# Kernel optimization log

Measured on AMD Instinct MI355X. Metric: run time of the kernel, lower is better.

The kernel has to match this reference:

```python
import jax, jax.numpy as jnp
import numpy as np

B, S, V, E, H, L = 128, 512, 32000, 256, 256, 9


def setup_inputs() -> dict:
    key = jax.random.key(0)
    ks = jax.random.split(key, 12)
    src_input = jax.random.randint(ks[0], (B, S), 0, V, dtype=jnp.int32)
    labels = jax.random.randint(ks[1], (B, S), 0, L, dtype=jnp.int32)
    masks = jnp.ones((B, S), dtype=bool)  # torchcrf requires mask[:, 0] all True
    g = lambda k, shape, s: (jax.random.normal(k, shape, jnp.float32) * s)
    inv = 1.0 / np.sqrt(H)
    return {
        "src_input": src_input,
        "labels": labels,
        "masks": masks,
        "embedding": g(ks[2], (V, E), 0.1),
        "W_ih": g(ks[3], (4 * H, E), inv),
        "W_hh": g(ks[4], (4 * H, H), inv),
        "b_ih": g(ks[5], (4 * H,), inv),
        "b_hh": g(ks[6], (4 * H,), inv),
        "W_lin": g(ks[7], (L, H), inv),
        "b_lin": g(ks[8], (L,), inv),
        "start_trans": g(ks[9], (L,), 0.1),
        "end_trans": g(ks[10], (L,), 0.1),
        "trans": g(ks[11], (L, L), 0.1),
    }


def _lstm(x, W_ih, W_hh, b_ih, b_hh):
    # x: [B,S,E] -> hidden states [B,S,H]; PyTorch gate order i,f,g,o
    b, s, _ = x.shape
    h_dim = W_hh.shape[1]
    xp = jnp.einsum('bse,ge->sbg', x, W_ih) + b_ih  # [S,B,4H] precomputed input proj

    def step(carry, xt):
        h, c = carry
        gates = xt + h @ W_hh.T + b_hh
        i, f, g, o = jnp.split(gates, 4, axis=-1)
        c = jax.nn.sigmoid(f) * c + jax.nn.sigmoid(i) * jnp.tanh(g)
        h = jax.nn.sigmoid(o) * jnp.tanh(c)
        return (h, c), h

    h0 = jnp.zeros((b, h_dim), x.dtype)
    _, hs = jax.lax.scan(step, (h0, h0), xp)  # [S,B,H]
    return jnp.swapaxes(hs, 0, 1)


def _crf_nll(emissions, labels, masks, start_trans, end_trans, trans):
    # torchcrf log-likelihood (reduction='sum'); model returns its negation
    maskf = masks.astype(emissions.dtype)
    lab = labels.astype(jnp.int32)
    # numerator: score of gold path
    em_tag = jnp.take_along_axis(emissions, lab[..., None], axis=2)[..., 0]  # [B,S]
    trans_sc = trans[lab[:, :-1], lab[:, 1:]]  # [B,S-1]
    score = start_trans[lab[:, 0]] + em_tag[:, 0]
    score = score + jnp.sum((trans_sc + em_tag[:, 1:]) * maskf[:, 1:], axis=1)
    seq_ends = jnp.sum(masks.astype(jnp.int32), axis=1) - 1
    last_tags = jnp.take_along_axis(lab, seq_ends[:, None], axis=1)[:, 0]
    score = score + end_trans[last_tags]
    # denominator: forward algorithm (log partition)
    alpha0 = start_trans + emissions[:, 0]  # [B,L]
    em_t = jnp.swapaxes(emissions, 0, 1)[1:]  # [S-1,B,L]
    m_t = jnp.swapaxes(masks, 0, 1)[1:]  # [S-1,B]

    def step(alpha, inp):
        e, m = inp
        nxt = jax.nn.logsumexp(alpha[:, :, None] + trans[None] + e[:, None, :], axis=1)
        return jnp.where(m[:, None], nxt, alpha), None

    alphaT, _ = jax.lax.scan(step, alpha0, (em_t, m_t))
    logZ = jax.nn.logsumexp(alphaT + end_trans, axis=1)  # [B]
    return -jnp.sum(score - logZ)


def reference(src_input, labels, masks, embedding, W_ih, W_hh, b_ih, b_hh,
              W_lin, b_lin, start_trans, end_trans, trans):
    x = embedding[src_input]  # [B,S,E]
    hs = _lstm(x, W_ih, W_hh, b_ih, b_hh)  # [B,S,H]; dropout is identity in eval
    emissions = jax.nn.relu(hs) @ W_lin.T + b_lin  # [B,S,L]
    return _crf_nll(emissions, labels, masks, start_trans, end_trans, trans)
```

## Files before the change

### kernel.cpp

```cpp
#include <hip/hip_runtime.h>
#include <hip/hip_fp16.h>
#include <stdint.h>

#define B_ 128
#define S_ 512
#define E_ 256
#define H_ 256
#define G_ 1024
#define L_ 9

#define NREG 45
#define NLDS 19
#define WREG_U4 (NREG * 512)
#define WTOT_U4 (WREG_U4 + NLDS * 512)

#define SM_H2   155648
#define SMEM2_TOTAL 156672

#define WS_W      0
#define WS_XP     (512 * 1024)
#define WS_HS     (WS_XP + (size_t)S_ * B_ * G_ * 2)
#define WS_EMB16  (WS_HS + (size_t)S_ * B_ * H_ * 2)
#define WS_WIH16  (WS_EMB16 + (size_t)32000 * E_ * 2)

typedef _Float16 f16x8v __attribute__((ext_vector_type(8)));
typedef float    f32x4v __attribute__((ext_vector_type(4)));

__device__ __forceinline__ uint32_t pack_f16x2(float a, float b) {
    __half2 h = __floats2half2_rn(a, b);
    union { __half2 h2; uint32_t u; } c;
    c.h2 = h;
    return c.u;
}

__device__ __forceinline__ float dot2h(uint32_t w, uint32_t h, float acc) {
#if __has_builtin(__builtin_amdgcn_fdot2)
    typedef _Float16 h2v __attribute__((ext_vector_type(2)));
    union { uint32_t u; h2v v; } uw, uh;
    uw.u = w; uh.u = h;
    return __builtin_amdgcn_fdot2(uw.v, uh.v, acc, false);
#else
    union { uint32_t u; __half2 h2; } uw, uh;
    uw.u = w; uh.u = h;
    float2 wf = __half22float2(uw.h2);
    float2 hf = __half22float2(uh.h2);
    return fmaf(wf.y, hf.y, fmaf(wf.x, hf.x, acc));
#endif
}

__device__ __forceinline__ float dot4h(uint4 w, uint4 h, float acc) {
    acc = dot2h(w.x, h.x, acc);
    acc = dot2h(w.y, h.y, acc);
    acc = dot2h(w.z, h.z, acc);
    acc = dot2h(w.w, h.w, acc);
    return acc;
}

__device__ __forceinline__ float sigm(float x)  { return 1.f / (1.f + __expf(-x)); }
__device__ __forceinline__ float tanh_f(float x){ return 1.f - 2.f / (__expf(2.f * x) + 1.f); }

__device__ __forceinline__ void lds_barrier() {
    asm volatile("s_waitcnt lgkmcnt(0)\n\ts_barrier" ::: "memory");
}

__global__ __launch_bounds__(256) void prep_weights(const float* __restrict__ W_hh,
                                                    uint4* __restrict__ W) {
    int idx = blockIdx.x * 256 + threadIdx.x;
    int l, w, q;
    if (idx < WREG_U4) {
        l = idx & 63; w = (idx >> 6) & 7; q = idx >> 9;
    } else {
        int r = idx - WREG_U4;
        l = r & 63; w = (r >> 6) & 7; q = NREG + (r >> 9);
    }
    int kt = q >> 3, nt = q & 7;
    int gate = nt & 3, jbl = nt >> 2;
    int jb = 2 * w + jbl;
    int row = gate * 256 + jb * 16 + (l & 15);
    int col = kt * 32 + (l >> 4) * 8;
    const float* p = W_hh + (size_t)row * H_ + col;
    uint4 v;
    v.x = pack_f16x2(p[0], p[1]);
    v.y = pack_f16x2(p[2], p[3]);
    v.z = pack_f16x2(p[4], p[5]);
    v.w = pack_f16x2(p[6], p[7]);
    W[idx] = v;
}

__global__ __launch_bounds__(256) void cvt_f16(const float* __restrict__ in,
                                               uint4* __restrict__ out, int n8) {
    int i = blockIdx.x * 256 + threadIdx.x;
    if (i >= n8) return;
    const float4* p = (const float4*)(in + (size_t)i * 8);
    float4 a = p[0], b = p[1];
    uint4 v;
    v.x = pack_f16x2(a.x, a.y);
    v.y = pack_f16x2(a.z, a.w);
    v.z = pack_f16x2(b.x, b.y);
    v.w = pack_f16x2(b.z, b.w);
    out[i] = v;
}

#define PADK 40
__global__ __launch_bounds__(256) void xp_gemm_mfma(
    const int* __restrict__ src, const __half* __restrict__ emb16,
    const __half* __restrict__ wih16, const float* __restrict__ b_ih,
    const float* __restrict__ b_hh, __half* __restrict__ xp16)
{
    __shared__ __align__(16) __half A_lds[64 * PADK];
    __shared__ __align__(16) __half Bt_lds[64 * PADK];
    __shared__ __align__(16) __half C_lds[64 * 72];
    __shared__ int tok[64];
    __shared__ float bias[64];

    int tid = threadIdx.x;
    int r0  = blockIdx.x * 64;
    int j0  = blockIdx.y * 16;

    if (tid < 64) {
        int r = r0 + tid;
        int tt = r >> 7, bb = r & 127;
        tok[tid] = src[bb * S_ + tt];
        int grow = (tid >> 4) * 256 + j0 + (tid & 15);
        bias[tid] = b_ih[grow] + b_hh[grow];
    }
    __syncthreads();

    int row = tid >> 2, q = tid & 3;
    const __half* arow = emb16 + (size_t)tok[row] * E_ + q * 8;
    int growb = (row >> 4) * 256 + j0 + (row & 15);
    const __half* brow = wih16 + (size_t)growb * E_ + q * 8;
    __half* asl = &A_lds[row * PADK + q * 8];
    __half* bsl = &Bt_lds[row * PADK + q * 8];

    int lane = tid & 63, w = tid >> 6;
    int ln = lane & 15, quad = lane >> 4;

    f32x4v acc0 = {0.f, 0.f, 0.f, 0.f};
    f32x4v acc1 = {0.f, 0.f, 0.f, 0.f};
    f32x4v acc2 = {0.f, 0.f, 0.f, 0.f};
    f32x4v acc3 = {0.f, 0.f, 0.f, 0.f};

    for (int kc = 0; kc < E_; kc += 32) {
        *(uint4*)asl = *(const uint4*)(arow + kc);
        *(uint4*)bsl = *(const uint4*)(brow + kc);
        __syncthreads();
        f16x8v af  = *(const f16x8v*)&A_lds[(w * 16 + ln) * PADK + quad * 8];
        f16x8v bf0 = *(const f16x8v*)&Bt_lds[(ln)      * PADK + quad * 8];
        f16x8v bf1 = *(const f16x8v*)&Bt_lds[(16 + ln) * PADK + quad * 8];
        f16x8v bf2 = *(const f16x8v*)&Bt_lds[(32 + ln) * PADK + quad * 8];
        f16x8v bf3 = *(const f16x8v*)&Bt_lds[(48 + ln) * PADK + quad * 8];
        acc0 = __builtin_amdgcn_mfma_f32_16x16x32_f16(af, bf0, acc0, 0, 0, 0);
        acc1 = __builtin_amdgcn_mfma_f32_16x16x32_f16(af, bf1, acc1, 0, 0, 0);
        acc2 = __builtin_amdgcn_mfma_f32_16x16x32_f16(af, bf2, acc2, 0, 0, 0);
        acc3 = __builtin_amdgcn_mfma_f32_16x16x32_f16(af, bf3, acc3, 0, 0, 0);
        __syncthreads();
    }

    #pragma unroll
    for (int nt = 0; nt < 4; ++nt) {
        f32x4v a = (nt == 0) ? acc0 : (nt == 1) ? acc1 : (nt == 2) ? acc2 : acc3;
        float bs = bias[nt * 16 + ln];
        #pragma unroll
        for (int reg = 0; reg < 4; ++reg) {
            int ml = w * 16 + quad * 4 + reg;
            C_lds[ml * 72 + ln * 4 + nt] = __float2half(a[reg] + bs);
        }
    }
    __syncthreads();

    int orow = tid >> 2, oc = tid & 3;
    uint4 vv = *(const uint4*)&C_lds[orow * 72 + oc * 16];
    *(uint4*)(xp16 + (size_t)(r0 + orow) * G_ + j0 * 4 + oc * 16) = vv;
}

__global__ __launch_bounds__(512, 2) void lstm_rec(
    const uint4* __restrict__ Wv, const __half* __restrict__ xp16,
    __half* __restrict__ hs)
{
    extern __shared__ char smem[];
    uint4*  wlds = (uint4*)smem;
    __half* hbuf = (__half*)(smem + SM_H2);

    int b    = blockIdx.x;
    int tid  = threadIdx.x;
    int l    = tid & 63, w = tid >> 6;
    int quad = l >> 4, ln = l & 15;

    f16x8v wr[NREG];
    #pragma unroll
    for (int q = 0; q < NREG; ++q)
        wr[q] = *(const f16x8v*)&Wv[q * 512 + tid];
    #pragma unroll
    for (int tl = 0; tl < NLDS; ++tl)
        wlds[w * (NLDS * 64) + tl * 64 + l] = Wv[WREG_U4 + tl * 512 + tid];

    if (tid < 256) hbuf[tid] = __float2half(0.f);
    __syncthreads();

    float c0 = 0.f, c1 = 0.f;
    const __half* xbase = xp16 + (size_t)b * G_;
    int j0 = 32 * w + ln;
    int j1 = j0 + 16;
    __half* ho = hs + (size_t)b * S_ * H_;
    const uint4* wp = wlds + (size_t)w * (NLDS * 64) + l;

    const f32x4v zz = {0.f, 0.f, 0.f, 0.f};
    uint2 xa = *(const uint2*)(xbase + j0 * 4);
    uint2 xb = *(const uint2*)(xbase + j0 * 4 + 64);

    for (int t = 0; t < S_; ++t) {
        int cur = t & 1, nxt = cur ^ 1;
        const __half* hb = hbuf + cur * 256 + quad * 8;

        f32x4v acc[8];
        #pragma unroll
        for (int kt = 0; kt < 8; ++kt) {
            f16x8v a = *(const f16x8v*)(hb + kt * 32);
            #pragma unroll
            for (int nt = 0; nt < 8; ++nt) {
                int q = kt * 8 + nt;
                f16x8v bf;
                if (q < NREG) bf = wr[q];
                else          bf = *(const f16x8v*)&wp[(q - NREG) * 64];
                f32x4v cin = (kt == 0) ? zz : acc[nt];
                acc[nt] = __builtin_amdgcn_mfma_f32_16x16x32_f16(a, bf, cin, 0, 0, 0);
            }
        }

        union { uint32_t u; __half2 h2; } u0, u1;
        u0.u = xa.x; u1.u = xa.y;
        float2 fa = __half22float2(u0.h2);
        float2 fb = __half22float2(u1.h2);
        float pi = acc[0][0] + fa.x, pf = acc[1][0] + fa.y;
        float pg = acc[2][0] + fb.x, po = acc[3][0] + fb.y;
        c0 = sigm(pf) * c0 + sigm(pi) * tanh_f(pg);
        float h0 = sigm(po) * tanh_f(c0);

        u0.u = xb.x; u1.u = xb.y;
        fa = __half22float2(u0.h2);
        fb = __half22float2(u1.h2);
        pi = acc[4][0] + fa.x; pf = acc[5][0] + fa.y;
        pg = acc[6][0] + fb.x; po = acc[7][0] + fb.y;
        c1 = sigm(pf) * c1 + sigm(pi) * tanh_f(pg);
        float h1 = sigm(po) * tanh_f(c1);

        if (quad == 0) {
            hbuf[nxt * 256 + j0] = __float2half(h0);
            hbuf[nxt * 256 + j1] = __float2half(h1);
        } else if (quad == 1) {
            ho[(size_t)t * H_ + j0] = __float2half(fmaxf(h0, 0.f));
            ho[(size_t)t * H_ + j1] = __float2half(fmaxf(h1, 0.f));
        }

        xbase += (size_t)B_ * G_;
        uint2 na = *(const uint2*)(xbase + j0 * 4);
        uint2 nb = *(const uint2*)(xbase + j0 * 4 + 64);

        lds_barrier();
        xa = na; xb = nb;
    }
}

__global__ __launch_bounds__(256) void emis_crf(
    const __half* __restrict__ hs, const int* __restrict__ labels,
    const float* __restrict__ W_lin, const float* __restrict__ b_lin,
    const float* __restrict__ start_trans, const float* __restrict__ end_trans,
    const float* __restrict__ trans, float* __restrict__ out)
{
    __shared__ uint32_t wlin2[L_ * 128];
    __shared__ float em_lds[S_ * 10];
    __shared__ int   lab_lds[S_];
    __shared__ float trans_lds[81];
    __shared__ float blin[L_], st_l[L_], en_l[L_];
    __shared__ float alpha_lds[2 * L_];

    int b = blockIdx.x, tid = threadIdx.x;

    for (int i = tid; i < L_ * 128; i += 256) {
        int l = i >> 7, k = i & 127;
        wlin2[i] = pack_f16x2(W_lin[l * H_ + 2 * k], W_lin[l * H_ + 2 * k + 1]);
    }
    if (tid < 81) trans_lds[tid] = trans[tid];
    if (tid < L_) { blin[tid] = b_lin[tid]; st_l[tid] = start_trans[tid]; en_l[tid] = end_trans[tid]; }
    lab_lds[tid]       = labels[b * S_ + tid];
    lab_lds[tid + 256] = labels[b * S_ + tid + 256];
    __syncthreads();

    const uint4* wl4 = (const uint4*)wlin2;
    #pragma unroll
    for (int r = 0; r < 2; ++r) {
        int t = tid + r * 256;
        const uint4* hr = (const uint4*)(hs + ((size_t)b * S_ + t) * H_);
        float acc[L_];
        #pragma unroll
        for (int l = 0; l < L_; ++l) acc[l] = blin[l];
        #pragma unroll
        for (int c = 0; c < 4; ++c) {
            uint4 hreg[8];
            #pragma unroll
            for (int k = 0; k < 8; ++k) hreg[k] = hr[c * 8 + k];
            #pragma unroll
            for (int l = 0; l < L_; ++l) {
                float a = acc[l];
                #pragma unroll
                for (int k = 0; k < 8; ++k)
                    a = dot4h(wl4[l * 32 + c * 8 + k], hreg[k], a);
                acc[l] = a;
            }
        }
        #pragma unroll
        for (int l = 0; l < L_; ++l) em_lds[t * 10 + l] = acc[l];
    }
    __syncthreads();

    if (tid < 16) {
        float score = 0.f;
        int prev_lab = 0;
        if (tid < L_) alpha_lds[tid] = st_l[tid] + em_lds[0 * 10 + tid];
        if (tid == 0) {
            int cl = lab_lds[0];
            prev_lab = cl;
            score = st_l[cl] + em_lds[0 * 10 + cl];
        }
        for (int t = 1; t < S_; ++t) {
            int cu = t & 1, pv = cu ^ 1;
            if (tid < L_) {
                float m = -1e30f;
                #pragma unroll
                for (int i2 = 0; i2 < L_; ++i2)
                    m = fmaxf(m, alpha_lds[pv * L_ + i2] + trans_lds[i2 * L_ + tid]);
                float s = 0.f;
                #pragma unroll
                for (int i2 = 0; i2 < L_; ++i2)
                    s += __expf(alpha_lds[pv * L_ + i2] + trans_lds[i2 * L_ + tid] - m);
                alpha_lds[cu * L_ + tid] = em_lds[t * 10 + tid] + m + __logf(s);
            }
            if (tid == 0) {
                int cl = lab_lds[t];
                score += trans_lds[prev_lab * L_ + cl] + em_lds[t * 10 + cl];
                prev_lab = cl;
            }
        }
        if (tid == 0) {
            int pv = (S_ - 1) & 1;
            float m = -1e30f;
            #pragma unroll
            for (int i2 = 0; i2 < L_; ++i2)
                m = fmaxf(m, alpha_lds[pv * L_ + i2] + en_l[i2]);
            float s = 0.f;
            #pragma unroll
            for (int i2 = 0; i2 < L_; ++i2)
                s += __expf(alpha_lds[pv * L_ + i2] + en_l[i2] - m);
            float logZ = m + __logf(s);
            score += en_l[prev_lab];
            atomicAdd(out, logZ - score);
        }
    }
}

extern "C" void kernel_launch(void* const* d_in, const int* in_sizes, int n_in,
                              void* d_out, int out_size, void* d_ws, size_t ws_size,
                              hipStream_t stream) {
    const int*   src         = (const int*)d_in[0];
    const int*   labels      = (const int*)d_in[1];
    const float* emb         = (const float*)d_in[3];
    const float* W_ih        = (const float*)d_in[4];
    const float* W_hh        = (const float*)d_in[5];
    const float* b_ih        = (const float*)d_in[6];
    const float* b_hh        = (const float*)d_in[7];
    const float* W_lin       = (const float*)d_in[8];
    const float* b_lin       = (const float*)d_in[9];
    const float* start_trans = (const float*)d_in[10];
    const float* end_trans   = (const float*)d_in[11];
    const float* trans       = (const float*)d_in[12];

    uint4*    W     = (uint4*)  ((char*)d_ws + WS_W);
    __half*   xp16  = (__half*) ((char*)d_ws + WS_XP);
    __half*   hsb   = (__half*) ((char*)d_ws + WS_HS);
    __half*   emb16 = (__half*) ((char*)d_ws + WS_EMB16);
    __half*   wih16 = (__half*) ((char*)d_ws + WS_WIH16);

    hipFuncSetAttribute((const void*)lstm_rec,
                        hipFuncAttributeMaxDynamicSharedMemorySize, SMEM2_TOTAL);

    hipMemsetAsync(d_out, 0, sizeof(float), stream);
    prep_weights<<<WTOT_U4 / 256, 256, 0, stream>>>(W_hh, W);
    cvt_f16<<<(32000 * E_ / 8 + 255) / 256, 256, 0, stream>>>(emb, (uint4*)emb16, 32000 * E_ / 8);
    cvt_f16<<<(G_ * E_ / 8 + 255) / 256, 256, 0, stream>>>(W_ih, (uint4*)wih16, G_ * E_ / 8);
    dim3 g1(1024, 16);
    xp_gemm_mfma<<<g1, 256, 0, stream>>>(src, emb16, wih16, b_ih, b_hh, xp16);
    lstm_rec<<<B_, 512, SMEM2_TOTAL, stream>>>(W, xp16, hsb);
    emis_crf<<<B_, 256, 0, stream>>>(hsb, labels, W_lin, b_lin,
                                     start_trans, end_trans, trans, (float*)d_out);
}
```

Measured before the change: 1.328 ms.

## Load full K tile once in xp GEMM, reorder LDS weights first in LSTM loop

The input-projection GEMM now stages the whole 256-wide K dimension of both A and B tiles into LDS in one pass. This replaces the per-32-column load/sync loop and cuts the barrier count, at the cost of more LDS per block, and launch bounds are set to request two blocks per CU. In the recurrent LSTM step, the weight fragments held in LDS are now mapped to the first k-tiles and the register-held ones to the later tiles, and the next h fragment is prefetched one k-tile ahead. This lets LDS latency overlap with the MFMA chain.

```diff
diff --git a/kernel.cpp b/kernel.cpp
--- a/kernel.cpp
+++ b/kernel.cpp
@@ -68,10 +68,10 @@
     int idx = blockIdx.x * 256 + threadIdx.x;
     int l, w, q;
     if (idx < WREG_U4) {
-        l = idx & 63; w = (idx >> 6) & 7; q = idx >> 9;
+        l = idx & 63; w = (idx >> 6) & 7; q = NLDS + (idx >> 9);
     } else {
         int r = idx - WREG_U4;
-        l = r & 63; w = (r >> 6) & 7; q = NREG + (r >> 9);
+        l = r & 63; w = (r >> 6) & 7; q = r >> 9;
     }
     int kt = q >> 3, nt = q & 7;
     int gate = nt & 3, jbl = nt >> 2;
@@ -101,14 +101,14 @@
     out[i] = v;
 }
 
-#define PADK 40
-__global__ __launch_bounds__(256) void xp_gemm_mfma(
+#define LDK 264
+__global__ __launch_bounds__(256, 2) void xp_gemm_mfma(
     const int* __restrict__ src, const __half* __restrict__ emb16,
     const __half* __restrict__ wih16, const float* __restrict__ b_ih,
     const float* __restrict__ b_hh, __half* __restrict__ xp16)
 {
-    __shared__ __align__(16) __half A_lds[64 * PADK];
-    __shared__ __align__(16) __half Bt_lds[64 * PADK];
+    __shared__ __align__(16) __half A_lds[64 * LDK];
+    __shared__ __align__(16) __half Bt_lds[64 * LDK];
     __shared__ __align__(16) __half C_lds[64 * 72];
     __shared__ int tok[64];
     __shared__ float bias[64];
@@ -126,12 +126,17 @@
     }
     __syncthreads();
 
-    int row = tid >> 2, q = tid & 3;
-    const __half* arow = emb16 + (size_t)tok[row] * E_ + q * 8;
-    int growb = (row >> 4) * 256 + j0 + (row & 15);
-    const __half* brow = wih16 + (size_t)growb * E_ + q * 8;
-    __half* asl = &A_lds[row * PADK + q * 8];
-    __half* bsl = &Bt_lds[row * PADK + q * 8];
+    #pragma unroll
+    for (int jl = 0; jl < 8; ++jl) {
+        int f = jl * 256 + tid;
+        int row = f >> 5, c16 = f & 31;
+        const uint4* ap = (const uint4*)(emb16 + (size_t)tok[row] * E_) + c16;
+        int growb = (row >> 4) * 256 + j0 + (row & 15);
+        const uint4* bp = (const uint4*)(wih16 + (size_t)growb * E_) + c16;
+        *(uint4*)&A_lds[row * LDK + c16 * 8]  = *ap;
+        *(uint4*)&Bt_lds[row * LDK + c16 * 8] = *bp;
+    }
+    __syncthreads();
 
     int lane = tid & 63, w = tid >> 6;
     int ln = lane & 15, quad = lane >> 4;
@@ -141,21 +146,20 @@
     f32x4v acc2 = {0.f, 0.f, 0.f, 0.f};
     f32x4v acc3 = {0.f, 0.f, 0.f, 0.f};
 
-    for (int kc = 0; kc < E_; kc += 32) {
-        *(uint4*)asl = *(const uint4*)(arow + kc);
-        *(uint4*)bsl = *(const uint4*)(brow + kc);
-        __syncthreads();
-        f16x8v af  = *(const f16x8v*)&A_lds[(w * 16 + ln) * PADK + quad * 8];
-        f16x8v bf0 = *(const f16x8v*)&Bt_lds[(ln)      * PADK + quad * 8];
-        f16x8v bf1 = *(const f16x8v*)&Bt_lds[(16 + ln) * PADK + quad * 8];
-        f16x8v bf2 = *(const f16x8v*)&Bt_lds[(32 + ln) * PADK + quad * 8];
-        f16x8v bf3 = *(const f16x8v*)&Bt_lds[(48 + ln) * PADK + quad * 8];
+    #pragma unroll
+    for (int kc = 0; kc < 8; ++kc) {
+        int ko = kc * 32 + quad * 8;
+        f16x8v af  = *(const f16x8v*)&A_lds[(w * 16 + ln) * LDK + ko];
+        f16x8v bf0 = *(const f16x8v*)&Bt_lds[(ln)      * LDK + ko];
+        f16x8v bf1 = *(const f16x8v*)&Bt_lds[(16 + ln) * LDK + ko];
+        f16x8v bf2 = *(const f16x8v*)&Bt_lds[(32 + ln) * LDK + ko];
+        f16x8v bf3 = *(const f16x8v*)&Bt_lds[(48 + ln) * LDK + ko];
         acc0 = __builtin_amdgcn_mfma_f32_16x16x32_f16(af, bf0, acc0, 0, 0, 0);
         acc1 = __builtin_amdgcn_mfma_f32_16x16x32_f16(af, bf1, acc1, 0, 0, 0);
         acc2 = __builtin_amdgcn_mfma_f32_16x16x32_f16(af, bf2, acc2, 0, 0, 0);
         acc3 = __builtin_amdgcn_mfma_f32_16x16x32_f16(af, bf3, acc3, 0, 0, 0);
-        __syncthreads();
-    }
+    }
+    __syncthreads();
 
     #pragma unroll
     for (int nt = 0; nt < 4; ++nt) {
@@ -214,18 +218,21 @@
         const __half* hb = hbuf + cur * 256 + quad * 8;
 
         f32x4v acc[8];
+        f16x8v a = *(const f16x8v*)(hb);
         #pragma unroll
         for (int kt = 0; kt < 8; ++kt) {
-            f16x8v a = *(const f16x8v*)(hb + kt * 32);
+            f16x8v anx = a;
+            if (kt < 7) anx = *(const f16x8v*)(hb + (kt + 1) * 32);
             #pragma unroll
             for (int nt = 0; nt < 8; ++nt) {
                 int q = kt * 8 + nt;
                 f16x8v bf;
-                if (q < NREG) bf = wr[q];
-                else          bf = *(const f16x8v*)&wp[(q - NREG) * 64];
+                if (q < NLDS) bf = *(const f16x8v*)&wp[q * 64];
+                else          bf = wr[q - NLDS];
                 f32x4v cin = (kt == 0) ? zz : acc[nt];
                 acc[nt] = __builtin_amdgcn_mfma_f32_16x16x32_f16(a, bf, cin, 0, 0, 0);
             }
+            a = anx;
         }
 
         union { uint32_t u; __half2 h2; } u0, u1;
```

Result: no change. 1.314 ms (-1.1%).
